# Performance work log

Hardware: AMD Instinct MI355X
Metric: run time of the kernel (lower is better)

## Reference

```python
import jax, jax.numpy as jnp
import numpy as np

NEG_NUM = -10000.0


def setup_inputs() -> dict:
    key = jax.random.key(0)
    k1, k2, k3 = jax.random.split(key, 3)
    B, S, T, D = 8, 4096, 512, 1024
    ctx = jax.random.normal(k1, (B, S, D), dtype=jnp.float32)
    query = jax.random.normal(k2, (B, T, D), dtype=jnp.float32)
    mask = jax.random.randint(k3, (B, S), 0, 2, dtype=jnp.int32)
    return {"ctx": ctx, "query": query, "mask": mask}


def reference(ctx, query, mask):
    # ctx: [B, S, D], query: [B, T, D], mask: [B, S] (0 = masked)
    D = query.shape[-1]
    denom = jnp.asarray(np.sqrt(D), dtype=ctx.dtype)
    # scores[b, t, s] = sum_d query[b, t, d] * ctx[b, s, d]
    scores = jnp.einsum("btd,bsd->bts", query, ctx) / denom
    # apply mask per source position (broadcast over target dim)
    scores = jnp.where(mask[:, None, :] == 0, NEG_NUM, scores)
    p_ctx = jax.nn.softmax(scores, axis=-1)  # [B, T, S]
    expected_ctx = jnp.einsum("bts,bsd->btd", p_ctx, ctx)  # [B, T, D]
    return expected_ctx, p_ctx
```

## Files before the change

kernel.cpp:

```cpp
#include <hip/hip_runtime.h>

#define BB 8
#define SS 4096
#define TT 512
#define DD 1024

typedef __attribute__((ext_vector_type(8))) short bf16x8;
typedef __attribute__((ext_vector_type(4))) short bf16x4;
typedef __attribute__((ext_vector_type(4))) float f32x4;

#define GLOAD_LDS16(gp, lp)                                            \
  __builtin_amdgcn_global_load_lds(                                    \
      (const __attribute__((address_space(1))) void*)(gp),             \
      (__attribute__((address_space(3))) void*)(lp), 16, 0, 0)

__device__ inline unsigned short f2bf(float f) {
  unsigned int u = __float_as_uint(f);
  u += 0x7FFFu + ((u >> 16) & 1u);
  return (unsigned short)(u >> 16);
}
__device__ inline void pack16(const float* __restrict__ src, short* __restrict__ dst) {
  f32x4 f0 = *(const f32x4*)(src + 0);
  f32x4 f1 = *(const f32x4*)(src + 4);
  f32x4 f2 = *(const f32x4*)(src + 8);
  f32x4 f3 = *(const f32x4*)(src + 12);
  bf16x8 b0, b1;
  b0[0] = (short)f2bf(f0.x); b0[1] = (short)f2bf(f0.y);
  b0[2] = (short)f2bf(f0.z); b0[3] = (short)f2bf(f0.w);
  b0[4] = (short)f2bf(f1.x); b0[5] = (short)f2bf(f1.y);
  b0[6] = (short)f2bf(f1.z); b0[7] = (short)f2bf(f1.w);
  b1[0] = (short)f2bf(f2.x); b1[1] = (short)f2bf(f2.y);
  b1[2] = (short)f2bf(f2.z); b1[3] = (short)f2bf(f2.w);
  b1[4] = (short)f2bf(f3.x); b1[5] = (short)f2bf(f3.y);
  b1[6] = (short)f2bf(f3.z); b1[7] = (short)f2bf(f3.w);
  *(bf16x8*)(dst + 0) = b0;
  *(bf16x8*)(dst + 8) = b1;
}

#define WS_NEED ((size_t)168 << 20)
#define OFF_QB  ((size_t)0)
#define OFF_CB  ((size_t)8 << 20)
#define OFF_CT  ((size_t)72 << 20)
#define OFF_PB  ((size_t)136 << 20)
#define OFF_PART ((size_t)0)

__global__ __launch_bounds__(256) void prep_q_kernel(const float* __restrict__ q,
                                                     short* __restrict__ qb) {
  const size_t idx = ((size_t)blockIdx.x * 256 + threadIdx.x) * 16;
  pack16(q + idx, qb + idx);
}

__global__ __launch_bounds__(256) void prep_c_kernel(const float* __restrict__ c,
                                                     short* __restrict__ cb,
                                                     short* __restrict__ ct) {
  const int b  = blockIdx.z;
  const int s0 = blockIdx.y * 64;
  const int d0 = blockIdx.x * 64;
  const float* C = c + (size_t)b * SS * DD;
  __shared__ float Tt[64][65];

  const int tid = threadIdx.x;
#pragma unroll
  for (int h = 0; h < 4; ++h) {
    const int sl = (tid >> 4) + h * 16;
    const int dl = (tid & 15) * 4;
    f32x4 v = *(const f32x4*)(C + (size_t)(s0 + sl) * DD + d0 + dl);
    *(f32x4*)&Tt[sl][dl] = v;
    bf16x4 o;
    o[0] = (short)f2bf(v.x); o[1] = (short)f2bf(v.y);
    o[2] = (short)f2bf(v.z); o[3] = (short)f2bf(v.w);
    *(bf16x4*)(cb + (size_t)b * SS * DD + (size_t)(s0 + sl) * DD + d0 + dl) = o;
  }
  __syncthreads();
#pragma unroll
  for (int g = 0; g < 2; ++g) {
    const int dl = (tid >> 3) + g * 32;
    const int sb = (tid & 7) * 8;
    bf16x8 o;
#pragma unroll
    for (int j = 0; j < 8; ++j) o[j] = (short)f2bf(Tt[sb + j][dl]);
    *(bf16x8*)(ct + (size_t)b * DD * SS + (size_t)(d0 + dl) * SS + s0 + sb) = o;
  }
}


__global__ __launch_bounds__(256) void qk_kernel_f(const short* __restrict__ qb,
                                                   const short* __restrict__ cb,
                                                   const int* __restrict__ mask,
                                                   float* __restrict__ p) {
  const int b  = blockIdx.z;
  const int m0 = blockIdx.y * 128;
  const int n0 = blockIdx.x * 128;
  const short* A  = qb + (size_t)b * TT * DD;
  const short* Bt = cb + (size_t)b * SS * DD;

  __shared__ alignas(16) short As[128 * 32];
  __shared__ alignas(16) short Bs[128 * 32];

  const int tid  = threadIdx.x;
  const int wave = tid >> 6, lane = tid & 63;
  const int quad = lane >> 4, l16 = lane & 15;
  const int wm = (wave >> 1) * 64, wn = (wave & 1) * 64;

  const int rl = lane >> 2;
  const int ck = (lane & 3) ^ ((lane >> 3) & 3);
  const int slot = (quad ^ ((l16 >> 1) & 3)) * 8;

  f32x4 acc[4][4];
#pragma unroll
  for (int i = 0; i < 4; ++i)
#pragma unroll
    for (int j = 0; j < 4; ++j) acc[i][j] = (f32x4){0.f, 0.f, 0.f, 0.f};

  for (int k0 = 0; k0 < DD; k0 += 32) {
    __syncthreads();
#pragma unroll
    for (int t = 0; t < 2; ++t) {
      const int rb = wave * 32 + t * 16;
      GLOAD_LDS16(A  + (size_t)(m0 + rb + rl) * DD + k0 + ck * 8, &As[rb * 32]);
      GLOAD_LDS16(Bt + (size_t)(n0 + rb + rl) * DD + k0 + ck * 8, &Bs[rb * 32]);
    }
    __syncthreads();

    bf16x8 af[4], bfv[4];
#pragma unroll
    for (int i = 0; i < 4; ++i)
      af[i] = *(const bf16x8*)&As[(wm + i * 16 + l16) * 32 + slot];
#pragma unroll
    for (int j = 0; j < 4; ++j)
      bfv[j] = *(const bf16x8*)&Bs[(wn + j * 16 + l16) * 32 + slot];
#pragma unroll
    for (int i = 0; i < 4; ++i)
#pragma unroll
      for (int j = 0; j < 4; ++j)
        acc[i][j] = __builtin_amdgcn_mfma_f32_16x16x32_bf16(af[i], bfv[j],
                                                            acc[i][j], 0, 0, 0);
  }

  float* P = p + (size_t)b * TT * SS;
  int mk[4];
#pragma unroll
  for (int j = 0; j < 4; ++j) mk[j] = mask[b * SS + n0 + wn + j * 16 + l16];
#pragma unroll
  for (int i = 0; i < 4; ++i)
#pragma unroll
    for (int j = 0; j < 4; ++j)
#pragma unroll
      for (int r = 0; r < 4; ++r) {
        const int row = m0 + wm + i * 16 + quad * 4 + r;
        const int col = n0 + wn + j * 16 + l16;
        const float val = (mk[j] == 0) ? -10000.0f : acc[i][j][r] * 0.03125f;
        P[(size_t)row * SS + col] = val;
      }
}

__global__ __launch_bounds__(256) void softmax_kernel_f(float* __restrict__ p,
                                                        short* __restrict__ pb) {
  const int row = blockIdx.x;
  float* pr = p + (size_t)row * SS;
  short* pbr = pb + (size_t)row * SS;
  const int tid = threadIdx.x;
  const int wave = tid >> 6, lane = tid & 63;

  float v[16];
  float mx = -3.0e38f;
#pragma unroll
  for (int h = 0; h < 4; ++h) {
    const int base = tid * 4 + h * 1024;
    f32x4 s = *(const f32x4*)(pr + base);
    v[h * 4 + 0] = s.x; v[h * 4 + 1] = s.y;
    v[h * 4 + 2] = s.z; v[h * 4 + 3] = s.w;
    mx = fmaxf(mx, fmaxf(fmaxf(s.x, s.y), fmaxf(s.z, s.w)));
  }
#pragma unroll
  for (int off = 32; off > 0; off >>= 1) mx = fmaxf(mx, __shfl_down(mx, off));
  __shared__ float red[4];
  if (lane == 0) red[wave] = mx;
  __syncthreads();
  mx = fmaxf(fmaxf(red[0], red[1]), fmaxf(red[2], red[3]));
  __syncthreads();

  float e[16];
  float sum = 0.f;
#pragma unroll
  for (int k = 0; k < 16; ++k) { e[k] = __expf(v[k] - mx); sum += e[k]; }
#pragma unroll
  for (int off = 32; off > 0; off >>= 1) sum += __shfl_down(sum, off);
  if (lane == 0) red[wave] = sum;
  __syncthreads();
  const float inv = 1.0f / (red[0] + red[1] + red[2] + red[3]);

#pragma unroll
  for (int h = 0; h < 4; ++h) {
    const int base = tid * 4 + h * 1024;
    f32x4 o;
    o.x = e[h * 4 + 0] * inv; o.y = e[h * 4 + 1] * inv;
    o.z = e[h * 4 + 2] * inv; o.w = e[h * 4 + 3] * inv;
    *(f32x4*)(pr + base) = o;
    bf16x4 ob;
    ob[0] = (short)f2bf(o.x); ob[1] = (short)f2bf(o.y);
    ob[2] = (short)f2bf(o.z); ob[3] = (short)f2bf(o.w);
    *(bf16x4*)(pbr + base) = ob;
  }
}

__global__ __launch_bounds__(256) void pv_kernel_f(const short* __restrict__ pb,
                                                   const short* __restrict__ ct,
                                                   float* __restrict__ part) {
  const int b  = blockIdx.z >> 2;
  const int ks = blockIdx.z & 3;
  const int m0 = blockIdx.y * 128;
  const int n0 = blockIdx.x * 128;
  const short* A  = pb + (size_t)b * TT * SS;
  const short* Bt = ct + (size_t)b * DD * SS;

  __shared__ alignas(16) short As[128 * 32];
  __shared__ alignas(16) short Bs[128 * 32];

  const int tid  = threadIdx.x;
  const int wave = tid >> 6, lane = tid & 63;
  const int quad = lane >> 4, l16 = lane & 15;
  const int wm = (wave >> 1) * 64, wn = (wave & 1) * 64;

  const int rl = lane >> 2;
  const int ck = (lane & 3) ^ ((lane >> 3) & 3);
  const int slot = (quad ^ ((l16 >> 1) & 3)) * 8;

  f32x4 acc[4][4];
#pragma unroll
  for (int i = 0; i < 4; ++i)
#pragma unroll
    for (int j = 0; j < 4; ++j) acc[i][j] = (f32x4){0.f, 0.f, 0.f, 0.f};

  const int kend = ks * 1024 + 1024;
  for (int k0 = ks * 1024; k0 < kend; k0 += 32) {
    __syncthreads();
#pragma unroll
    for (int t = 0; t < 2; ++t) {
      const int rb = wave * 32 + t * 16;
      GLOAD_LDS16(A  + (size_t)(m0 + rb + rl) * SS + k0 + ck * 8, &As[rb * 32]);
      GLOAD_LDS16(Bt + (size_t)(n0 + rb + rl) * SS + k0 + ck * 8, &Bs[rb * 32]);
    }
    __syncthreads();

    bf16x8 af[4], bfv[4];
#pragma unroll
    for (int i = 0; i < 4; ++i)
      af[i] = *(const bf16x8*)&As[(wm + i * 16 + l16) * 32 + slot];
#pragma unroll
    for (int j = 0; j < 4; ++j)
      bfv[j] = *(const bf16x8*)&Bs[(wn + j * 16 + l16) * 32 + slot];
#pragma unroll
    for (int i = 0; i < 4; ++i)
#pragma unroll
      for (int j = 0; j < 4; ++j)
        acc[i][j] = __builtin_amdgcn_mfma_f32_16x16x32_bf16(af[i], bfv[j],
                                                            acc[i][j], 0, 0, 0);
  }

  float* E = part + (size_t)ks * BB * TT * DD + (size_t)b * TT * DD;
#pragma unroll
  for (int i = 0; i < 4; ++i)
#pragma unroll
    for (int j = 0; j < 4; ++j)
#pragma unroll
      for (int r = 0; r < 4; ++r) {
        const int row = m0 + wm + i * 16 + quad * 4 + r;
        const int col = n0 + wn + j * 16 + l16;
        E[(size_t)row * DD + col] = acc[i][j][r];
      }
}

__global__ __launch_bounds__(256) void reduce_kernel(const float* __restrict__ part,
                                                     float* __restrict__ e) {
  const size_t idx = ((size_t)blockIdx.x * 256 + threadIdx.x) * 4;
  const size_t N = (size_t)BB * TT * DD;
  f32x4 a0 = *(const f32x4*)(part + idx);
  f32x4 a1 = *(const f32x4*)(part + N + idx);
  f32x4 a2 = *(const f32x4*)(part + 2 * N + idx);
  f32x4 a3 = *(const f32x4*)(part + 3 * N + idx);
  f32x4 o;
  o.x = (a0.x + a1.x) + (a2.x + a3.x);
  o.y = (a0.y + a1.y) + (a2.y + a3.y);
  o.z = (a0.z + a1.z) + (a2.z + a3.z);
  o.w = (a0.w + a1.w) + (a2.w + a3.w);
  *(f32x4*)(e + idx) = o;
}

__global__ __launch_bounds__(256) void qk_kernel(const float* __restrict__ q,
                                                 const float* __restrict__ c,
                                                 float* __restrict__ p) {
  const int b  = blockIdx.z;
  const int m0 = blockIdx.y * 128;
  const int n0 = blockIdx.x * 128;
  const float* A  = q + (size_t)b * TT * DD;
  const float* Bt = c + (size_t)b * SS * DD;
  __shared__ alignas(16) short As[128 * 40];
  __shared__ alignas(16) short Bs[128 * 40];
  const int tid  = threadIdx.x;
  const int wave = tid >> 6, lane = tid & 63;
  const int quad = lane >> 4, l16 = lane & 15;
  const int wm = (wave >> 1) * 64, wn = (wave & 1) * 64;
  f32x4 acc[4][4];
#pragma unroll
  for (int i = 0; i < 4; ++i)
#pragma unroll
    for (int j = 0; j < 4; ++j) acc[i][j] = (f32x4){0.f, 0.f, 0.f, 0.f};
  const int ar = tid >> 1;
  const int ak = (tid & 1) * 16;
  for (int k0 = 0; k0 < DD; k0 += 32) {
    __syncthreads();
    pack16(A  + (size_t)(m0 + ar) * DD + k0 + ak, &As[ar * 40 + ak]);
    pack16(Bt + (size_t)(n0 + ar) * DD + k0 + ak, &Bs[ar * 40 + ak]);
    __syncthreads();
    bf16x8 af[4], bfv[4];
#pragma unroll
    for (int i = 0; i < 4; ++i)
      af[i] = *(const bf16x8*)&As[(wm + i * 16 + l16) * 40 + quad * 8];
#pragma unroll
    for (int j = 0; j < 4; ++j)
      bfv[j] = *(const bf16x8*)&Bs[(wn + j * 16 + l16) * 40 + quad * 8];
#pragma unroll
    for (int i = 0; i < 4; ++i)
#pragma unroll
      for (int j = 0; j < 4; ++j)
        acc[i][j] = __builtin_amdgcn_mfma_f32_16x16x32_bf16(af[i], bfv[j],
                                                            acc[i][j], 0, 0, 0);
  }
  float* P = p + (size_t)b * TT * SS;
#pragma unroll
  for (int i = 0; i < 4; ++i)
#pragma unroll
    for (int j = 0; j < 4; ++j)
#pragma unroll
      for (int r = 0; r < 4; ++r) {
        const int row = m0 + wm + i * 16 + quad * 4 + r;
        const int col = n0 + wn + j * 16 + l16;
        P[(size_t)row * SS + col] = acc[i][j][r] * 0.03125f;
      }
}

__global__ __launch_bounds__(256) void softmax_kernel(float* __restrict__ p,
                                                      const int* __restrict__ mask) {
  const int row = blockIdx.x;
  const int b   = row >> 9;
  float* pr = p + (size_t)row * SS;
  const int* mr = mask + b * SS;
  const int tid = threadIdx.x;
  const int wave = tid >> 6, lane = tid & 63;
  float v[16];
  float mx = -3.0e38f;
#pragma unroll
  for (int h = 0; h < 4; ++h) {
    const int base = tid * 4 + h * 1024;
    f32x4 s = *(const f32x4*)(pr + base);
    const int4 m4 = *(const int4*)(mr + base);
#pragma unroll
    for (int j = 0; j < 4; ++j) {
      float f = (j == 0 ? s.x : j == 1 ? s.y : j == 2 ? s.z : s.w);
      const int mk = (j == 0 ? m4.x : j == 1 ? m4.y : j == 2 ? m4.z : m4.w);
      f = fminf(fmaxf(f, -1.0e30f), 1.0e30f);
      f = (mk == 0) ? -10000.0f : f;
      v[h * 4 + j] = f;
      mx = fmaxf(mx, f);
    }
  }
#pragma unroll
  for (int off = 32; off > 0; off >>= 1) mx = fmaxf(mx, __shfl_down(mx, off));
  __shared__ float red[4];
  if (lane == 0) red[wave] = mx;
  __syncthreads();
  mx = fmaxf(fmaxf(red[0], red[1]), fmaxf(red[2], red[3]));
  __syncthreads();
  float e[16];
  float sum = 0.f;
#pragma unroll
  for (int k = 0; k < 16; ++k) { e[k] = __expf(v[k] - mx); sum += e[k]; }
#pragma unroll
  for (int off = 32; off > 0; off >>= 1) sum += __shfl_down(sum, off);
  if (lane == 0) red[wave] = sum;
  __syncthreads();
  const float inv = 1.0f / (red[0] + red[1] + red[2] + red[3]);
#pragma unroll
  for (int h = 0; h < 4; ++h) {
    const int base = tid * 4 + h * 1024;
    f32x4 o;
    o.x = e[h * 4 + 0] * inv; o.y = e[h * 4 + 1] * inv;
    o.z = e[h * 4 + 2] * inv; o.w = e[h * 4 + 3] * inv;
    *(f32x4*)(pr + base) = o;
  }
}

__global__ __launch_bounds__(256) void pv_kernel(const float* __restrict__ p,
                                                 const float* __restrict__ c,
                                                 float* __restrict__ e) {
  const int b  = blockIdx.z;
  const int m0 = blockIdx.y * 128;
  const int n0 = blockIdx.x * 128;
  const float* A  = p + (size_t)b * TT * SS;
  const float* Bm = c + (size_t)b * SS * DD;
  __shared__ alignas(16) short As[128 * 40];
  __shared__ alignas(16) short Bs[128 * 40];
  const int tid  = threadIdx.x;
  const int wave = tid >> 6, lane = tid & 63;
  const int quad = lane >> 4, l16 = lane & 15;
  const int wm = (wave >> 1) * 64, wn = (wave & 1) * 64;
  f32x4 acc[4][4];
#pragma unroll
  for (int i = 0; i < 4; ++i)
#pragma unroll
    for (int j = 0; j < 4; ++j) acc[i][j] = (f32x4){0.f, 0.f, 0.f, 0.f};
  const int ar = tid >> 1;
  const int ak = (tid & 1) * 16;
  const int kk = tid >> 3;
  const int c0 = (tid & 7) * 16;
  for (int k0 = 0; k0 < SS; k0 += 32) {
    __syncthreads();
    pack16(A + (size_t)(m0 + ar) * SS + k0 + ak, &As[ar * 40 + ak]);
    {
      const float* bp = Bm + (size_t)(k0 + kk) * DD + n0 + c0;
#pragma unroll
      for (int h = 0; h < 4; ++h) {
        f32x4 f = *(const f32x4*)(bp + h * 4);
        Bs[(c0 + h * 4 + 0) * 40 + kk] = (short)f2bf(f.x);
        Bs[(c0 + h * 4 + 1) * 40 + kk] = (short)f2bf(f.y);
        Bs[(c0 + h * 4 + 2) * 40 + kk] = (short)f2bf(f.z);
        Bs[(c0 + h * 4 + 3) * 40 + kk] = (short)f2bf(f.w);
      }
    }
    __syncthreads();
    bf16x8 af[4], bfv[4];
#pragma unroll
    for (int i = 0; i < 4; ++i)
      af[i] = *(const bf16x8*)&As[(wm + i * 16 + l16) * 40 + quad * 8];
#pragma unroll
    for (int j = 0; j < 4; ++j)
      bfv[j] = *(const bf16x8*)&Bs[(wn + j * 16 + l16) * 40 + quad * 8];
#pragma unroll
    for (int i = 0; i < 4; ++i)
#pragma unroll
      for (int j = 0; j < 4; ++j)
        acc[i][j] = __builtin_amdgcn_mfma_f32_16x16x32_bf16(af[i], bfv[j],
                                                            acc[i][j], 0, 0, 0);
  }
  float* E = e + (size_t)b * TT * DD;
#pragma unroll
  for (int i = 0; i < 4; ++i)
#pragma unroll
    for (int j = 0; j < 4; ++j)
#pragma unroll
      for (int r = 0; r < 4; ++r) {
        const int row = m0 + wm + i * 16 + quad * 4 + r;
        const int col = n0 + wn + j * 16 + l16;
        E[(size_t)row * DD + col] = acc[i][j][r];
      }
}

extern "C" void kernel_launch(void* const* d_in, const int* in_sizes, int n_in,
                              void* d_out, int out_size, void* d_ws, size_t ws_size,
                              hipStream_t stream) {
  const float* ctx   = (const float*)d_in[0];
  const float* query = (const float*)d_in[1];
  const int*   mask  = (const int*)d_in[2];

  float* expected = (float*)d_out;
  float* p        = (float*)d_out + (size_t)BB * TT * DD;

  if (ws_size >= WS_NEED) {
    char* ws = (char*)d_ws;
    short* qb = (short*)(ws + OFF_QB);
    short* cb = (short*)(ws + OFF_CB);
    short* ct = (short*)(ws + OFF_CT);
    short* pb = (short*)(ws + OFF_PB);
    float* part = (float*)(ws + OFF_PART);

    prep_q_kernel<<<dim3((BB * TT * DD) / (256 * 16)), 256, 0, stream>>>(query, qb);
    prep_c_kernel<<<dim3(DD / 64, SS / 64, BB), 256, 0, stream>>>(ctx, cb, ct);
    qk_kernel_f<<<dim3(SS / 128, TT / 128, BB), 256, 0, stream>>>(qb, cb, mask, p);
    softmax_kernel_f<<<dim3(BB * TT), 256, 0, stream>>>(p, pb);
    pv_kernel_f<<<dim3(DD / 128, TT / 128, BB * 4), 256, 0, stream>>>(pb, ct, part);
    reduce_kernel<<<dim3((BB * TT * DD) / (256 * 4)), 256, 0, stream>>>(part, expected);
  } else {
    qk_kernel<<<dim3(SS / 128, TT / 128, BB), 256, 0, stream>>>(query, ctx, p);
    softmax_kernel<<<dim3(BB * TT), 256, 0, stream>>>(p, mask);
    pv_kernel<<<dim3(DD / 128, TT / 128, BB), 256, 0, stream>>>(p, ctx, expected);
  }
}
```

Before: 422.1 us.

## Enlarge ctx transpose tiles, swizzle block order, halve PV split-K

The ctx prep kernel now handles 128x128 tiles and transposes the already-converted bf16 values through shared memory, writing 16-byte rows of the transposed copy. The QK and PV GEMMs remap block IDs with an XCD-style swizzle so neighbouring tiles run on the same chiplet and share L2. PV split-K drops from 4 to 2, so the reduce kernel reads half as many partials. Fewer PV blocks may underfill the GPU (256 blocks), and the strided 2-byte LDS writes in the transpose can cause bank conflicts.

```diff
diff --git a/kernel.cpp b/kernel.cpp
--- a/kernel.cpp
+++ b/kernel.cpp
@@ -8,6 +8,7 @@
 typedef __attribute__((ext_vector_type(8))) short bf16x8;
 typedef __attribute__((ext_vector_type(4))) short bf16x4;
 typedef __attribute__((ext_vector_type(4))) float f32x4;
+typedef __attribute__((ext_vector_type(4))) unsigned int u32x4;
 
 #define GLOAD_LDS16(gp, lp)                                            \
   __builtin_amdgcn_global_load_lds(                                    \
@@ -54,32 +55,40 @@
                                                      short* __restrict__ cb,
                                                      short* __restrict__ ct) {
   const int b  = blockIdx.z;
-  const int s0 = blockIdx.y * 64;
-  const int d0 = blockIdx.x * 64;
+  const int s0 = blockIdx.y * 128;
+  const int d0 = blockIdx.x * 128;
   const float* C = c + (size_t)b * SS * DD;
-  __shared__ float Tt[64][65];
+  __shared__ alignas(16) short T[128 * 130];
 
   const int tid = threadIdx.x;
-#pragma unroll
-  for (int h = 0; h < 4; ++h) {
-    const int sl = (tid >> 4) + h * 16;
-    const int dl = (tid & 15) * 4;
-    f32x4 v = *(const f32x4*)(C + (size_t)(s0 + sl) * DD + d0 + dl);
-    *(f32x4*)&Tt[sl][dl] = v;
+  const int sl = tid >> 5;
+  const int dl = (tid & 31) * 4;
+#pragma unroll
+  for (int h = 0; h < 16; ++h) {
+    const int s = sl + h * 8;
+    f32x4 v = *(const f32x4*)(C + (size_t)(s0 + s) * DD + d0 + dl);
     bf16x4 o;
     o[0] = (short)f2bf(v.x); o[1] = (short)f2bf(v.y);
     o[2] = (short)f2bf(v.z); o[3] = (short)f2bf(v.w);
-    *(bf16x4*)(cb + (size_t)b * SS * DD + (size_t)(s0 + sl) * DD + d0 + dl) = o;
-  }
-  __syncthreads();
-#pragma unroll
-  for (int g = 0; g < 2; ++g) {
-    const int dl = (tid >> 3) + g * 32;
-    const int sb = (tid & 7) * 8;
-    bf16x8 o;
-#pragma unroll
-    for (int j = 0; j < 8; ++j) o[j] = (short)f2bf(Tt[sb + j][dl]);
-    *(bf16x8*)(ct + (size_t)b * DD * SS + (size_t)(d0 + dl) * SS + s0 + sb) = o;
+    *(bf16x4*)(cb + (size_t)b * SS * DD + (size_t)(s0 + s) * DD + d0 + dl) = o;
+    T[(dl + 0) * 130 + s] = o[0];
+    T[(dl + 1) * 130 + s] = o[1];
+    T[(dl + 2) * 130 + s] = o[2];
+    T[(dl + 3) * 130 + s] = o[3];
+  }
+  __syncthreads();
+  const int dr = tid >> 4;
+  const int sc = (tid & 15) * 8;
+#pragma unroll
+  for (int g = 0; g < 8; ++g) {
+    const int d = dr + g * 16;
+    const int base = d * 130 + sc;
+    u32x4 w;
+    w.x = *(const unsigned int*)&T[base + 0];
+    w.y = *(const unsigned int*)&T[base + 2];
+    w.z = *(const unsigned int*)&T[base + 4];
+    w.w = *(const unsigned int*)&T[base + 6];
+    *(u32x4*)(ct + (size_t)b * DD * SS + (size_t)(d0 + d) * SS + s0 + sc) = w;
   }
 }
 
@@ -88,9 +97,11 @@
                                                    const short* __restrict__ cb,
                                                    const int* __restrict__ mask,
                                                    float* __restrict__ p) {
-  const int b  = blockIdx.z;
-  const int m0 = blockIdx.y * 128;
-  const int n0 = blockIdx.x * 128;
+  const int bid = blockIdx.x + 32 * (blockIdx.y + 4 * blockIdx.z);
+  const int swz = (bid & 7) * 128 + (bid >> 3);
+  const int n0 = (swz & 31) * 128;
+  const int m0 = ((swz >> 5) & 3) * 128;
+  const int b  = swz >> 7;
   const short* A  = qb + (size_t)b * TT * DD;
   const short* Bt = cb + (size_t)b * SS * DD;
 
@@ -207,10 +218,13 @@
 __global__ __launch_bounds__(256) void pv_kernel_f(const short* __restrict__ pb,
                                                    const short* __restrict__ ct,
                                                    float* __restrict__ part) {
-  const int b  = blockIdx.z >> 2;
-  const int ks = blockIdx.z & 3;
-  const int m0 = blockIdx.y * 128;
-  const int n0 = blockIdx.x * 128;
+  const int bid = blockIdx.x + 8 * (blockIdx.y + 4 * blockIdx.z);
+  const int swz = (bid & 7) * 64 + (bid >> 3);
+  const int n0 = (swz & 7) * 128;
+  const int m0 = ((swz >> 3) & 3) * 128;
+  const int z  = swz >> 5;
+  const int b  = z >> 1;
+  const int ks = z & 1;
   const short* A  = pb + (size_t)b * TT * SS;
   const short* Bt = ct + (size_t)b * DD * SS;
 
@@ -232,8 +246,8 @@
 #pragma unroll
     for (int j = 0; j < 4; ++j) acc[i][j] = (f32x4){0.f, 0.f, 0.f, 0.f};
 
-  const int kend = ks * 1024 + 1024;
-  for (int k0 = ks * 1024; k0 < kend; k0 += 32) {
+  const int kend = ks * 2048 + 2048;
+  for (int k0 = ks * 2048; k0 < kend; k0 += 32) {
     __syncthreads();
 #pragma unroll
     for (int t = 0; t < 2; ++t) {
@@ -277,13 +291,11 @@
   const size_t N = (size_t)BB * TT * DD;
   f32x4 a0 = *(const f32x4*)(part + idx);
   f32x4 a1 = *(const f32x4*)(part + N + idx);
-  f32x4 a2 = *(const f32x4*)(part + 2 * N + idx);
-  f32x4 a3 = *(const f32x4*)(part + 3 * N + idx);
   f32x4 o;
-  o.x = (a0.x + a1.x) + (a2.x + a3.x);
-  o.y = (a0.y + a1.y) + (a2.y + a3.y);
-  o.z = (a0.z + a1.z) + (a2.z + a3.z);
-  o.w = (a0.w + a1.w) + (a2.w + a3.w);
+  o.x = a0.x + a1.x;
+  o.y = a0.y + a1.y;
+  o.z = a0.z + a1.z;
+  o.w = a0.w + a1.w;
   *(f32x4*)(e + idx) = o;
 }
 
@@ -475,10 +487,10 @@
     float* part = (float*)(ws + OFF_PART);
 
     prep_q_kernel<<<dim3((BB * TT * DD) / (256 * 16)), 256, 0, stream>>>(query, qb);
-    prep_c_kernel<<<dim3(DD / 64, SS / 64, BB), 256, 0, stream>>>(ctx, cb, ct);
+    prep_c_kernel<<<dim3(DD / 128, SS / 128, BB), 256, 0, stream>>>(ctx, cb, ct);
     qk_kernel_f<<<dim3(SS / 128, TT / 128, BB), 256, 0, stream>>>(qb, cb, mask, p);
     softmax_kernel_f<<<dim3(BB * TT), 256, 0, stream>>>(p, pb);
-    pv_kernel_f<<<dim3(DD / 128, TT / 128, BB * 4), 256, 0, stream>>>(pb, ct, part);
+    pv_kernel_f<<<dim3(DD / 128, TT / 128, BB * 2), 256, 0, stream>>>(pb, ct, part);
     reduce_kernel<<<dim3((BB * TT * DD) / (256 * 4)), 256, 0, stream>>>(part, expected);
   } else {
     qk_kernel<<<dim3(SS / 128, TT / 128, BB), 256, 0, stream>>>(query, ctx, p);
```

Result: slower. 435.0 us (+3.1%).

## Swizzle GEMM block order, use wave-per-row softmax, halve PV split-K

Applied to the files above, without the earlier changes.

The QK and PV GEMM kernels now remap their block index with an XCD-aware swizzle, so that consecutive blocks on each chiplet share operand tiles in L2. The softmax kernel assigns one wave per row and uses xor-shuffle reductions, which removes the LDS traffic and barriers. PV split-K goes from 4 to 2, which halves the partial-sum writes and the work in the reduce kernel but gives PV half as many blocks. These are several independent tweaks across three kernels.

```diff
diff --git a/kernel.cpp b/kernel.cpp
--- a/kernel.cpp
+++ b/kernel.cpp
@@ -88,9 +88,11 @@
                                                    const short* __restrict__ cb,
                                                    const int* __restrict__ mask,
                                                    float* __restrict__ p) {
-  const int b  = blockIdx.z;
-  const int m0 = blockIdx.y * 128;
-  const int n0 = blockIdx.x * 128;
+  const int bid = blockIdx.x + 32 * (blockIdx.y + 4 * blockIdx.z);
+  const int swz = (bid & 7) * 128 + (bid >> 3);
+  const int n0 = (swz & 31) * 128;
+  const int m0 = ((swz >> 5) & 3) * 128;
+  const int b  = swz >> 7;
   const short* A  = qb + (size_t)b * TT * DD;
   const short* Bt = cb + (size_t)b * SS * DD;
 
@@ -156,61 +158,57 @@
 
 __global__ __launch_bounds__(256) void softmax_kernel_f(float* __restrict__ p,
                                                         short* __restrict__ pb) {
-  const int row = blockIdx.x;
+  const int wave = threadIdx.x >> 6, lane = threadIdx.x & 63;
+  const int row = blockIdx.x * 4 + wave;
   float* pr = p + (size_t)row * SS;
   short* pbr = pb + (size_t)row * SS;
-  const int tid = threadIdx.x;
-  const int wave = tid >> 6, lane = tid & 63;
-
-  float v[16];
+
+  f32x4 v[16];
   float mx = -3.0e38f;
 #pragma unroll
-  for (int h = 0; h < 4; ++h) {
-    const int base = tid * 4 + h * 1024;
-    f32x4 s = *(const f32x4*)(pr + base);
-    v[h * 4 + 0] = s.x; v[h * 4 + 1] = s.y;
-    v[h * 4 + 2] = s.z; v[h * 4 + 3] = s.w;
-    mx = fmaxf(mx, fmaxf(fmaxf(s.x, s.y), fmaxf(s.z, s.w)));
-  }
-#pragma unroll
-  for (int off = 32; off > 0; off >>= 1) mx = fmaxf(mx, __shfl_down(mx, off));
-  __shared__ float red[4];
-  if (lane == 0) red[wave] = mx;
-  __syncthreads();
-  mx = fmaxf(fmaxf(red[0], red[1]), fmaxf(red[2], red[3]));
-  __syncthreads();
-
-  float e[16];
+  for (int h = 0; h < 16; ++h) {
+    v[h] = *(const f32x4*)(pr + h * 256 + lane * 4);
+    mx = fmaxf(mx, fmaxf(fmaxf(v[h].x, v[h].y), fmaxf(v[h].z, v[h].w)));
+  }
+#pragma unroll
+  for (int off = 32; off > 0; off >>= 1) mx = fmaxf(mx, __shfl_xor(mx, off));
+
   float sum = 0.f;
 #pragma unroll
-  for (int k = 0; k < 16; ++k) { e[k] = __expf(v[k] - mx); sum += e[k]; }
-#pragma unroll
-  for (int off = 32; off > 0; off >>= 1) sum += __shfl_down(sum, off);
-  if (lane == 0) red[wave] = sum;
-  __syncthreads();
-  const float inv = 1.0f / (red[0] + red[1] + red[2] + red[3]);
-
-#pragma unroll
-  for (int h = 0; h < 4; ++h) {
-    const int base = tid * 4 + h * 1024;
+  for (int h = 0; h < 16; ++h) {
+    v[h].x = __expf(v[h].x - mx);
+    v[h].y = __expf(v[h].y - mx);
+    v[h].z = __expf(v[h].z - mx);
+    v[h].w = __expf(v[h].w - mx);
+    sum += (v[h].x + v[h].y) + (v[h].z + v[h].w);
+  }
+#pragma unroll
+  for (int off = 32; off > 0; off >>= 1) sum += __shfl_xor(sum, off);
+  const float inv = 1.0f / sum;
+
+#pragma unroll
+  for (int h = 0; h < 16; ++h) {
     f32x4 o;
-    o.x = e[h * 4 + 0] * inv; o.y = e[h * 4 + 1] * inv;
-    o.z = e[h * 4 + 2] * inv; o.w = e[h * 4 + 3] * inv;
-    *(f32x4*)(pr + base) = o;
+    o.x = v[h].x * inv; o.y = v[h].y * inv;
+    o.z = v[h].z * inv; o.w = v[h].w * inv;
+    *(f32x4*)(pr + h * 256 + lane * 4) = o;
     bf16x4 ob;
     ob[0] = (short)f2bf(o.x); ob[1] = (short)f2bf(o.y);
     ob[2] = (short)f2bf(o.z); ob[3] = (short)f2bf(o.w);
-    *(bf16x4*)(pbr + base) = ob;
+    *(bf16x4*)(pbr + h * 256 + lane * 4) = ob;
   }
 }
 
 __global__ __launch_bounds__(256) void pv_kernel_f(const short* __restrict__ pb,
                                                    const short* __restrict__ ct,
                                                    float* __restrict__ part) {
-  const int b  = blockIdx.z >> 2;
-  const int ks = blockIdx.z & 3;
-  const int m0 = blockIdx.y * 128;
-  const int n0 = blockIdx.x * 128;
+  const int bid = blockIdx.x + 8 * (blockIdx.y + 4 * blockIdx.z);
+  const int swz = (bid & 7) * 64 + (bid >> 3);
+  const int n0 = (swz & 7) * 128;
+  const int m0 = ((swz >> 3) & 3) * 128;
+  const int z  = swz >> 5;
+  const int b  = z >> 1;
+  const int ks = z & 1;
   const short* A  = pb + (size_t)b * TT * SS;
   const short* Bt = ct + (size_t)b * DD * SS;
 
@@ -232,8 +230,8 @@
 #pragma unroll
     for (int j = 0; j < 4; ++j) acc[i][j] = (f32x4){0.f, 0.f, 0.f, 0.f};
 
-  const int kend = ks * 1024 + 1024;
-  for (int k0 = ks * 1024; k0 < kend; k0 += 32) {
+  const int kend = ks * 2048 + 2048;
+  for (int k0 = ks * 2048; k0 < kend; k0 += 32) {
     __syncthreads();
 #pragma unroll
     for (int t = 0; t < 2; ++t) {
@@ -277,13 +275,11 @@
   const size_t N = (size_t)BB * TT * DD;
   f32x4 a0 = *(const f32x4*)(part + idx);
   f32x4 a1 = *(const f32x4*)(part + N + idx);
-  f32x4 a2 = *(const f32x4*)(part + 2 * N + idx);
-  f32x4 a3 = *(const f32x4*)(part + 3 * N + idx);
   f32x4 o;
-  o.x = (a0.x + a1.x) + (a2.x + a3.x);
-  o.y = (a0.y + a1.y) + (a2.y + a3.y);
-  o.z = (a0.z + a1.z) + (a2.z + a3.z);
-  o.w = (a0.w + a1.w) + (a2.w + a3.w);
+  o.x = a0.x + a1.x;
+  o.y = a0.y + a1.y;
+  o.z = a0.z + a1.z;
+  o.w = a0.w + a1.w;
   *(f32x4*)(e + idx) = o;
 }
 
@@ -315,7 +311,7 @@
     __syncthreads();
     bf16x8 af[4], bfv[4];
 #pragma unroll
-    for (int i = 0; i < 4; ++i)
+  for (int i = 0; i < 4; ++i)
       af[i] = *(const bf16x8*)&As[(wm + i * 16 + l16) * 40 + quad * 8];
 #pragma unroll
     for (int j = 0; j < 4; ++j)
@@ -477,8 +473,8 @@
     prep_q_kernel<<<dim3((BB * TT * DD) / (256 * 16)), 256, 0, stream>>>(query, qb);
     prep_c_kernel<<<dim3(DD / 64, SS / 64, BB), 256, 0, stream>>>(ctx, cb, ct);
     qk_kernel_f<<<dim3(SS / 128, TT / 128, BB), 256, 0, stream>>>(qb, cb, mask, p);
-    softmax_kernel_f<<<dim3(BB * TT), 256, 0, stream>>>(p, pb);
-    pv_kernel_f<<<dim3(DD / 128, TT / 128, BB * 4), 256, 0, stream>>>(pb, ct, part);
+    softmax_kernel_f<<<dim3((BB * TT) / 4), 256, 0, stream>>>(p, pb);
+    pv_kernel_f<<<dim3(DD / 128, TT / 128, BB * 2), 256, 0, stream>>>(pb, ct, part);
     reduce_kernel<<<dim3((BB * TT * DD) / (256 * 4)), 256, 0, stream>>>(part, expected);
   } else {
     qk_kernel<<<dim3(SS / 128, TT / 128, BB), 256, 0, stream>>>(query, ctx, p);
```

After: 424.5 us. Within noise of the previous version (+0.6%).
